# Kernel tuning notes

Measured on AMD Instinct MI355X. Metric: run time of the kernel, lower is better.

## Reference

```python
import jax, jax.numpy as jnp
import numpy as np

B, L, Q = 1024, 200, 1
DQ, DF = 512, 128
H, D1, D2 = 4, 128, 64


def setup_inputs() -> dict:
    key = jax.random.key(0)
    ks = jax.random.split(key, 20)
    inp = {
        "query": jax.random.normal(ks[0], (B, Q, DQ), jnp.float32),
        "fact": jax.random.normal(ks[1], (B, L, DF), jnp.float32),
        "mask": jax.random.randint(ks[2], (B, L), 0, 2, jnp.int32),
        "mm_cosine": jax.random.normal(ks[3], (2, B, L), jnp.float32),
    }
    # per-head FCRepeat weights, init per reset_parameters: randn/sqrt(fan_in), bias 0.1
    def w(k, fan_in, fan_out):
        return jax.random.normal(k, (H, fan_in, fan_out), jnp.float32) / np.sqrt(fan_in).astype(np.float32)
    inp["Wq1"] = w(ks[4], DQ, D1); inp["bq1"] = jnp.full((H, D1), 0.1, jnp.float32)
    inp["Wq2"] = w(ks[5], D1, D2); inp["bq2"] = jnp.full((H, D2), 0.1, jnp.float32)
    inp["Wf1"] = w(ks[6], DF, D1); inp["bf1"] = jnp.full((H, D1), 0.1, jnp.float32)
    inp["Wf2"] = w(ks[7], D1, D2); inp["bf2"] = jnp.full((H, D2), 0.1, jnp.float32)
    inp["Wv1"] = w(ks[8], DF, D1); inp["bv1"] = jnp.full((H, D1), 0.1, jnp.float32)
    inp["Wv2"] = w(ks[9], D1, D2); inp["bv2"] = jnp.full((H, D2), 0.1, jnp.float32)
    inp["tau1"] = jnp.full((2, H), 0.1, jnp.float32)   # cosine_tau1
    inp["tau2"] = jnp.full((3, H), 1.0, jnp.float32)   # cosine_tau2
    return inp


def _silu(x):
    return x * jax.nn.sigmoid(x)


def reference(query, fact, mask, mm_cosine,
              Wq1, bq1, Wq2, bq2, Wf1, bf1, Wf2, bf2, Wv1, bv1, Wv2, bv2,
              tau1, tau2):
    # per-head FC stacks (identity acts inside FCRepeat), then SiLU gating
    fq = jnp.einsum('bqi,hio->hbqo', query, Wq1) + bq1[:, None, None, :]
    fq = jnp.einsum('hbqi,hio->hbqo', fq, Wq2) + bq2[:, None, None, :]
    fq = _silu(fq)                                   # [H,B,1,D2]
    ff = jnp.einsum('bli,hio->hblo', fact, Wf1) + bf1[:, None, None, :]
    ff = jnp.einsum('hbli,hio->hblo', ff, Wf2) + bf2[:, None, None, :]
    ff = _silu(ff)                                   # [H,B,L,D2]
    fv = jnp.einsum('bli,hio->hblo', fact, Wv1) + bv1[:, None, None, :]
    fv = jnp.einsum('hbli,hio->hblo', fv, Wv2) + bv2[:, None, None, :]
    fv = _silu(fv)                                   # [H,B,L,D2]

    dot = jnp.einsum('hbld,hbqd->hblq', ff, fq)      # [H,B,L,1]
    dot = dot + (-1e9) * (1.0 - mask.astype(jnp.float32))[None, :, :, None]

    # cosine-bias cross terms
    bias = (mm_cosine[0][None] / tau1[0][:, None, None]
            + mm_cosine[1][None] / tau1[1][:, None, None])[..., None]  # [H,B,L,1]
    b1, b2, b3 = (tau2[i][:, None, None, None] for i in range(3))
    dot = b1 * dot + b2 * bias + b3 * dot * bias

    alphas = jax.nn.softmax(dot, axis=2) + 1e-7      # softmax over L
    out = jnp.einsum('hbld,hblq->hbdq', fv, alphas)[..., 0]  # [H,B,D2]
    return jnp.transpose(out, (1, 0, 2)).reshape(out.shape[1], -1)  # [B,H*D2]
```

## Files before the change

kernel.cpp:

```cpp
#include <hip/hip_runtime.h>
#include <hip/hip_bf16.h>

typedef __attribute__((ext_vector_type(8))) short short8;
typedef __attribute__((ext_vector_type(4))) float f32x4;

#define NH   4
#define NB   1024
#define NL   200
#define NDQ  512
#define NDF  128
#define ND1  128
#define ND2  64
#define LPAD 208
#define KP   136

#define OFF_WQC   0
#define OFF_BQC   (NH*NDQ*ND2*4)
#define OFF_FQ    (OFF_BQC + NH*ND2*4)
#define OFF_WIMG  (OFF_FQ + NH*NB*ND2*4)
#define OFF_BFC   (OFF_WIMG + NH*3*ND2*KP*2)
#define OFF_BVC   (OFF_BFC + NH*ND2*4)

__device__ inline short f2bf(float f) {
    union { float f; unsigned u; } v; v.f = f;
    unsigned r = (v.u + 0x7FFFu + ((v.u >> 16) & 1u)) >> 16;
    return (short)r;
}
__device__ inline float bf2f(short s) {
    union { unsigned u; float f; } v; v.u = ((unsigned)(unsigned short)s) << 16;
    return v.f;
}

__global__ __launch_bounds__(256) void k_combine(
    const float* __restrict__ Wq1, const float* __restrict__ bq1,
    const float* __restrict__ Wq2, const float* __restrict__ bq2,
    const float* __restrict__ Wf1, const float* __restrict__ bf1,
    const float* __restrict__ Wf2, const float* __restrict__ bf2,
    const float* __restrict__ Wv1, const float* __restrict__ bv1,
    const float* __restrict__ Wv2, const float* __restrict__ bv2,
    float* __restrict__ WQC, float* __restrict__ BQC,
    __hip_bfloat16* __restrict__ WIMG, float* __restrict__ BFC, float* __restrict__ BVC)
{
    int g = blockIdx.x * 256 + threadIdx.x;
    if (g < NH*NDQ*ND2) {
        int h = g >> 15, r = g & 32767, i = r >> 6, j = r & 63;
        const float* a  = Wq1 + (h*NDQ + i)*ND1;
        const float* bb = Wq2 + h*ND1*ND2 + j;
        float s = 0.f;
        for (int k = 0; k < ND1; ++k) s += a[k] * bb[k*ND2];
        WQC[(h*NDQ + i)*ND2 + j] = s;
        return;
    }
    g -= NH*NDQ*ND2;
    if (g < 2*NH*NDF*ND2) {
        int which = (g >= NH*NDF*ND2);
        int r0 = g & (NH*NDF*ND2 - 1);
        int h = r0 >> 13, r = r0 & 8191, i = r >> 6, j = r & 63;
        const float* W1 = (which ? Wv1 : Wf1) + (h*NDF + i)*ND1;
        const float* W2 = (which ? Wv2 : Wf2) + h*ND1*ND2 + j;
        float s = 0.f;
        for (int k = 0; k < ND1; ++k) s += W1[k] * W2[k*ND2];
        short hi = f2bf(s);
        short lo = f2bf(s - bf2f(hi));
        __hip_bfloat16* img = WIMG + (size_t)((h*3 + (which ? 2 : 0))*ND2 + j)*KP + i;
        ((short*)img)[0] = hi;
        if (!which) ((short*)img)[ND2*KP] = lo;
        return;
    }
    g -= 2*NH*NDF*ND2;
    if (g < NH*ND2) {
        int h = g >> 6, j = g & 63;
        float s = bq2[h*ND2 + j];
        for (int k = 0; k < ND1; ++k) s += bq1[h*ND1 + k] * Wq2[(h*ND1 + k)*ND2 + j];
        BQC[g] = s; return;
    }
    g -= NH*ND2;
    if (g < NH*ND2) {
        int h = g >> 6, j = g & 63;
        float s = bf2[h*ND2 + j];
        for (int k = 0; k < ND1; ++k) s += bf1[h*ND1 + k] * Wf2[(h*ND1 + k)*ND2 + j];
        BFC[g] = s; return;
    }
    g -= NH*ND2;
    if (g < NH*ND2) {
        int h = g >> 6, j = g & 63;
        float s = bv2[h*ND2 + j];
        for (int k = 0; k < ND1; ++k) s += bv1[h*ND1 + k] * Wv2[(h*ND1 + k)*ND2 + j];
        BVC[g] = s; return;
    }
}

__global__ __launch_bounds__(256) void k_fq(
    const float* __restrict__ query, const float* __restrict__ WQC,
    const float* __restrict__ BQC, float* __restrict__ FQ)
{
    __shared__ __align__(16) float qS[8*NDQ];
    const int t = threadIdx.x;
    const int b0 = blockIdx.x * 8;
    {
        const float4* src = (const float4*)(query + (size_t)b0 * NDQ);
        float4* dst = (float4*)qS;
        for (int i = t; i < 8*NDQ/4; i += 256) dst[i] = src[i];
    }
    __syncthreads();
    const int h = t >> 6, d = t & 63;
    float s[8];
    {
        float b = BQC[h*ND2 + d];
        for (int g = 0; g < 8; ++g) s[g] = b;
    }
    const float* wp = WQC + (size_t)h*NDQ*ND2 + d;
    for (int i = 0; i < NDQ; ++i) {
        float w = wp[i*ND2];
        for (int g = 0; g < 8; ++g) s[g] += qS[g*NDQ + i] * w;
    }
    for (int g = 0; g < 8; ++g) {
        float v = s[g];
        FQ[((size_t)h*NB + b0 + g)*ND2 + d] = v / (1.f + expf(-v));
    }
}

__global__ __launch_bounds__(512, 2) void k_main(
    const float* __restrict__ fact,
    const int* __restrict__ mask,
    const float* __restrict__ mmc,
    const float* __restrict__ tau1,
    const float* __restrict__ tau2,
    const float* __restrict__ FQ,
    const float* __restrict__ BFC,
    const float* __restrict__ BVC,
    const __hip_bfloat16* __restrict__ WIMG,
    float* __restrict__ out)
{
    __shared__ __align__(16) __hip_bfloat16 wS[2*ND2*KP];
    __shared__ __align__(16) float dotS[LPAD];
    __shared__ __align__(16) float alphaS[LPAD];
    __shared__ __align__(16) float redS[8];
    __shared__ __align__(16) float outPartS[512];

    const int t    = threadIdx.x;
    const int b    = blockIdx.x;
    const int w    = t >> 6;
    const int lane = t & 63;
    const int a15  = lane & 15;
    const int quad = lane >> 4;
    const int nmt  = (w < 5) ? 2 : 1;

    short8 afh[2][4], afl[2][4];
    const short8 zero8 = {0,0,0,0,0,0,0,0};
    for (int mi = 0; mi < 2; ++mi) {
        int mt = w + 8*mi;
        int row = mt*16 + a15;
        for (int kk = 0; kk < 4; ++kk) {
            short8 vh = zero8, vl = zero8;
            if (mt < 13 && row < NL) {
                const float* p = fact + ((size_t)(b*NL + row))*NDF + kk*32 + quad*8;
                float4 x0 = *(const float4*)p;
                float4 x1 = *(const float4*)(p + 4);
                float v[8] = {x0.x, x0.y, x0.z, x0.w, x1.x, x1.y, x1.z, x1.w};
                for (int j = 0; j < 8; ++j) {
                    short hs = f2bf(v[j]);
                    vh[j] = hs;
                    vl[j] = f2bf(v[j] - bf2f(hs));
                }
            }
            afh[mi][kk] = vh;
            afl[mi][kk] = vl;
        }
    }

    const int bL = b * NL;
    const f32x4 zf = {0.f, 0.f, 0.f, 0.f};

    for (int h = 0; h < NH; ++h) {
        __syncthreads();
        {
            const float4* src = (const float4*)(WIMG + (size_t)(h*3)*ND2*KP);
            float4* dst = (float4*)wS;
            for (int i = t; i < 2176; i += 512) dst[i] = src[i];
        }
        float fqv[4], bfcv[4], bvcv[4];
        for (int nt = 0; nt < 4; ++nt) {
            int col = nt*16 + a15;
            fqv[nt]  = FQ[((size_t)h*NB + b)*ND2 + col];
            bfcv[nt] = BFC[h*ND2 + col];
            bvcv[nt] = BVC[h*ND2 + col];
        }
        const float t1a = tau1[h];
        const float t1b = tau1[NH + h];
        const float t20 = tau2[h];
        const float t21 = tau2[NH + h];
        const float t22 = tau2[2*NH + h];
        __syncthreads();

        f32x4 acc[2][4];
        for (int mi = 0; mi < 2; ++mi) for (int nt = 0; nt < 4; ++nt) acc[mi][nt] = zf;
        for (int kk = 0; kk < 4; ++kk) {
            short8 bh[4], bl[4];
            for (int nt = 0; nt < 4; ++nt) {
                const __hip_bfloat16* p = wS + (nt*16 + a15)*KP + kk*32 + quad*8;
                bh[nt] = *(const short8*)p;
                bl[nt] = *(const short8*)(p + ND2*KP);
            }
            for (int mi = 0; mi < 2; ++mi)
                if (mi < nmt)
                    for (int nt = 0; nt < 4; ++nt) {
                        acc[mi][nt] = __builtin_amdgcn_mfma_f32_16x16x32_bf16(afh[mi][kk], bh[nt], acc[mi][nt], 0, 0, 0);
                        acc[mi][nt] = __builtin_amdgcn_mfma_f32_16x16x32_bf16(afh[mi][kk], bl[nt], acc[mi][nt], 0, 0, 0);
                        acc[mi][nt] = __builtin_amdgcn_mfma_f32_16x16x32_bf16(afl[mi][kk], bh[nt], acc[mi][nt], 0, 0, 0);
                    }
        }

        for (int mi = 0; mi < 2; ++mi)
            if (mi < nmt) {
                int mt = w + 8*mi;
                for (int rg = 0; rg < 4; ++rg) {
                    float s = 0.f;
                    for (int nt = 0; nt < 4; ++nt) {
                        float z = acc[mi][nt][rg] + bfcv[nt];
                        float ffv = z / (1.f + expf(-z));
                        s += ffv * fqv[nt];
                    }
                    s += __shfl_xor(s, 1);
                    s += __shfl_xor(s, 2);
                    s += __shfl_xor(s, 4);
                    s += __shfl_xor(s, 8);
                    if (a15 == rg) dotS[mt*16 + quad*4 + rg] = s;
                }
            }
        __syncthreads();

        {
            const float4* src = (const float4*)(WIMG + (size_t)(h*3 + 2)*ND2*KP);
            float4* dst = (float4*)wS;
            for (int i = t; i < 1088; i += 512) dst[i] = src[i];
        }

        float logit = -3.0e38f;
        float e = 0.f;
        if (t < NL) {
            float dv = dotS[t] - 1e9f * (1.0f - (float)mask[bL + t]);
            float bias = mmc[bL + t] / t1a + mmc[NB*NL + bL + t] / t1b;
            logit = t20*dv + t21*bias + t22*dv*bias;
        }
        float vmax = logit;
        for (int off = 1; off < 64; off <<= 1) vmax = fmaxf(vmax, __shfl_xor(vmax, off));
        if (lane == 0) redS[w] = vmax;
        __syncthreads();
        vmax = redS[0];
        for (int i = 1; i < 8; ++i) vmax = fmaxf(vmax, redS[i]);
        if (t < NL) e = expf(logit - vmax);
        float vsum = e;
        for (int off = 1; off < 64; off <<= 1) vsum += __shfl_xor(vsum, off);
        __syncthreads();
        if (lane == 0) redS[w] = vsum;
        __syncthreads();
        vsum = 0.f;
        for (int i = 0; i < 8; ++i) vsum += redS[i];
        if (t < LPAD) alphaS[t] = (t < NL) ? (e / vsum + 1e-7f) : 0.f;
        __syncthreads();

        for (int mi = 0; mi < 2; ++mi) for (int nt = 0; nt < 4; ++nt) acc[mi][nt] = zf;
        for (int kk = 0; kk < 4; ++kk) {
            short8 bh[4];
            for (int nt = 0; nt < 4; ++nt)
                bh[nt] = *(const short8*)(wS + (nt*16 + a15)*KP + kk*32 + quad*8);
            for (int mi = 0; mi < 2; ++mi)
                if (mi < nmt)
                    for (int nt = 0; nt < 4; ++nt)
                        acc[mi][nt] = __builtin_amdgcn_mfma_f32_16x16x32_bf16(afh[mi][kk], bh[nt], acc[mi][nt], 0, 0, 0);
        }

        float o[4] = {0.f, 0.f, 0.f, 0.f};
        for (int mi = 0; mi < 2; ++mi)
            if (mi < nmt) {
                int mt = w + 8*mi;
                const f32x4 al = *(const f32x4*)(alphaS + mt*16 + quad*4);
                for (int rg = 0; rg < 4; ++rg)
                    for (int nt = 0; nt < 4; ++nt) {
                        float z = acc[mi][nt][rg] + bvcv[nt];
                        float fvv = z / (1.f + expf(-z));
                        o[nt] += al[rg] * fvv;
                    }
            }
        for (int nt = 0; nt < 4; ++nt) {
            o[nt] += __shfl_xor(o[nt], 16);
            o[nt] += __shfl_xor(o[nt], 32);
        }
        if (lane < 16)
            for (int nt = 0; nt < 4; ++nt) outPartS[w*64 + nt*16 + lane] = o[nt];
        __syncthreads();
        if (t < 64) {
            float s = 0.f;
            for (int ww = 0; ww < 8; ++ww) s += outPartS[ww*64 + t];
            out[(size_t)b*(NH*ND2) + h*ND2 + t] = s;
        }
    }
}

extern "C" void kernel_launch(void* const* d_in, const int* in_sizes, int n_in,
                              void* d_out, int out_size, void* d_ws, size_t ws_size,
                              hipStream_t stream) {
    const float* query = (const float*)d_in[0];
    const float* fact  = (const float*)d_in[1];
    const int*   maskp = (const int*)d_in[2];
    const float* mmc   = (const float*)d_in[3];
    const float* Wq1 = (const float*)d_in[4];
    const float* bq1 = (const float*)d_in[5];
    const float* Wq2 = (const float*)d_in[6];
    const float* bq2 = (const float*)d_in[7];
    const float* Wf1 = (const float*)d_in[8];
    const float* bf1 = (const float*)d_in[9];
    const float* Wf2 = (const float*)d_in[10];
    const float* bf2 = (const float*)d_in[11];
    const float* Wv1 = (const float*)d_in[12];
    const float* bv1 = (const float*)d_in[13];
    const float* Wv2 = (const float*)d_in[14];
    const float* bv2 = (const float*)d_in[15];
    const float* tau1 = (const float*)d_in[16];
    const float* tau2 = (const float*)d_in[17];

    char* ws = (char*)d_ws;
    float*          WQC  = (float*)(ws + OFF_WQC);
    float*          BQC  = (float*)(ws + OFF_BQC);
    float*          FQ   = (float*)(ws + OFF_FQ);
    __hip_bfloat16* WIMG = (__hip_bfloat16*)(ws + OFF_WIMG);
    float*          BFC  = (float*)(ws + OFF_BFC);
    float*          BVC  = (float*)(ws + OFF_BVC);

    k_combine<<<771, 256, 0, stream>>>(Wq1, bq1, Wq2, bq2, Wf1, bf1, Wf2, bf2,
                                       Wv1, bv1, Wv2, bv2, WQC, BQC, WIMG, BFC, BVC);
    k_fq<<<NB/8, 256, 0, stream>>>(query, WQC, BQC, FQ);
    k_main<<<NB, 512, 0, stream>>>(fact, maskp, mmc, tau1, tau2, FQ, BFC, BVC, WIMG,
                                   (float*)d_out);
}
```

Baseline: 417.5 us.

## Cut barriers in main kernel by loading all weights once and wave-local softmax

```diff
diff --git a/kernel.cpp b/kernel.cpp
--- a/kernel.cpp
+++ b/kernel.cpp
@@ -29,6 +29,9 @@
 __device__ inline float bf2f(short s) {
     union { unsigned u; float f; } v; v.u = ((unsigned)(unsigned short)s) << 16;
     return v.f;
+}
+__device__ inline float fsilu(float z) {
+    return z * __fdividef(1.f, 1.f + __expf(-z));
 }
 
 __global__ __launch_bounds__(256) void k_combine(
@@ -94,30 +97,33 @@
     const float* __restrict__ query, const float* __restrict__ WQC,
     const float* __restrict__ BQC, float* __restrict__ FQ)
 {
-    __shared__ __align__(16) float qS[8*NDQ];
+    __shared__ __align__(16) float qS[4*NDQ];
     const int t = threadIdx.x;
-    const int b0 = blockIdx.x * 8;
+    const int b0 = blockIdx.x * 4;
     {
         const float4* src = (const float4*)(query + (size_t)b0 * NDQ);
         float4* dst = (float4*)qS;
-        for (int i = t; i < 8*NDQ/4; i += 256) dst[i] = src[i];
+        dst[t] = src[t];
+        dst[t + 256] = src[t + 256];
     }
     __syncthreads();
     const int h = t >> 6, d = t & 63;
-    float s[8];
-    {
-        float b = BQC[h*ND2 + d];
-        for (int g = 0; g < 8; ++g) s[g] = b;
-    }
+    float s0, s1, s2, s3;
+    s0 = s1 = s2 = s3 = BQC[h*ND2 + d];
     const float* wp = WQC + (size_t)h*NDQ*ND2 + d;
+    #pragma unroll 8
     for (int i = 0; i < NDQ; ++i) {
-        float w = wp[i*ND2];
-        for (int g = 0; g < 8; ++g) s[g] += qS[g*NDQ + i] * w;
-    }
-    for (int g = 0; g < 8; ++g) {
-        float v = s[g];
-        FQ[((size_t)h*NB + b0 + g)*ND2 + d] = v / (1.f + expf(-v));
-    }
+        float wv = wp[i*ND2];
+        s0 += qS[i]        * wv;
+        s1 += qS[NDQ + i]  * wv;
+        s2 += qS[2*NDQ + i]* wv;
+        s3 += qS[3*NDQ + i]* wv;
+    }
+    float* o = FQ + ((size_t)h*NB + b0)*ND2 + d;
+    o[0]      = fsilu(s0);
+    o[ND2]    = fsilu(s1);
+    o[2*ND2]  = fsilu(s2);
+    o[3*ND2]  = fsilu(s3);
 }
 
 __global__ __launch_bounds__(512, 2) void k_main(
@@ -132,10 +138,8 @@
     const __hip_bfloat16* __restrict__ WIMG,
     float* __restrict__ out)
 {
-    __shared__ __align__(16) __hip_bfloat16 wS[2*ND2*KP];
+    __shared__ __align__(16) __hip_bfloat16 wS[3*ND2*KP];
     __shared__ __align__(16) float dotS[LPAD];
-    __shared__ __align__(16) float alphaS[LPAD];
-    __shared__ __align__(16) float redS[8];
     __shared__ __align__(16) float outPartS[512];
 
     const int t    = threadIdx.x;
@@ -174,10 +178,15 @@
 
     for (int h = 0; h < NH; ++h) {
         __syncthreads();
+        if (h > 0 && t < 64) {
+            float s = 0.f;
+            for (int ww = 0; ww < 8; ++ww) s += outPartS[ww*64 + t];
+            out[(size_t)b*(NH*ND2) + (h-1)*ND2 + t] = s;
+        }
         {
             const float4* src = (const float4*)(WIMG + (size_t)(h*3)*ND2*KP);
             float4* dst = (float4*)wS;
-            for (int i = t; i < 2176; i += 512) dst[i] = src[i];
+            for (int i = t; i < 3264; i += 512) dst[i] = src[i];
         }
         float fqv[4], bfcv[4], bvcv[4];
         for (int nt = 0; nt < 4; ++nt) {
@@ -216,11 +225,8 @@
                 int mt = w + 8*mi;
                 for (int rg = 0; rg < 4; ++rg) {
                     float s = 0.f;
-                    for (int nt = 0; nt < 4; ++nt) {
-                        float z = acc[mi][nt][rg] + bfcv[nt];
-                        float ffv = z / (1.f + expf(-z));
-                        s += ffv * fqv[nt];
-                    }
+                    for (int nt = 0; nt < 4; ++nt)
+                        s += fsilu(acc[mi][nt][rg] + bfcv[nt]) * fqv[nt];
                     s += __shfl_xor(s, 1);
                     s += __shfl_xor(s, 2);
                     s += __shfl_xor(s, 4);
@@ -230,41 +236,51 @@
             }
         __syncthreads();
 
-        {
-            const float4* src = (const float4*)(WIMG + (size_t)(h*3 + 2)*ND2*KP);
-            float4* dst = (float4*)wS;
-            for (int i = t; i < 1088; i += 512) dst[i] = src[i];
-        }
-
-        float logit = -3.0e38f;
-        float e = 0.f;
-        if (t < NL) {
-            float dv = dotS[t] - 1e9f * (1.0f - (float)mask[bL + t]);
-            float bias = mmc[bL + t] / t1a + mmc[NB*NL + bL + t] / t1b;
-            logit = t20*dv + t21*bias + t22*dv*bias;
-        }
-        float vmax = logit;
+        float lg[4];
+        float vmax = -3.0e38f;
+        #pragma unroll
+        for (int j = 0; j < 4; ++j) {
+            int r = lane + 64*j;
+            float l = -3.0e38f;
+            if (r < NL) {
+                float dv = dotS[r] - 1e9f * (1.0f - (float)mask[bL + r]);
+                float bias = __fdividef(mmc[bL + r], t1a) + __fdividef(mmc[NB*NL + bL + r], t1b);
+                l = t20*dv + t21*bias + t22*dv*bias;
+            }
+            lg[j] = l;
+            vmax = fmaxf(vmax, l);
+        }
+        #pragma unroll
         for (int off = 1; off < 64; off <<= 1) vmax = fmaxf(vmax, __shfl_xor(vmax, off));
-        if (lane == 0) redS[w] = vmax;
-        __syncthreads();
-        vmax = redS[0];
-        for (int i = 1; i < 8; ++i) vmax = fmaxf(vmax, redS[i]);
-        if (t < NL) e = expf(logit - vmax);
-        float vsum = e;
+        float vsum = 0.f;
+        #pragma unroll
+        for (int j = 0; j < 4; ++j)
+            if (lane + 64*j < NL) vsum += __expf(lg[j] - vmax);
+        #pragma unroll
         for (int off = 1; off < 64; off <<= 1) vsum += __shfl_xor(vsum, off);
-        __syncthreads();
-        if (lane == 0) redS[w] = vsum;
-        __syncthreads();
-        vsum = 0.f;
-        for (int i = 0; i < 8; ++i) vsum += redS[i];
-        if (t < LPAD) alphaS[t] = (t < NL) ? (e / vsum + 1e-7f) : 0.f;
-        __syncthreads();
+        const float rdenom = __fdividef(1.f, vsum);
+
+        float al[2][4];
+        for (int mi = 0; mi < 2; ++mi)
+            for (int rg = 0; rg < 4; ++rg) {
+                float a = 0.f;
+                if (mi < nmt) {
+                    int r = (w + 8*mi)*16 + quad*4 + rg;
+                    if (r < NL) {
+                        float dv = dotS[r] - 1e9f * (1.0f - (float)mask[bL + r]);
+                        float bias = __fdividef(mmc[bL + r], t1a) + __fdividef(mmc[NB*NL + bL + r], t1b);
+                        float l = t20*dv + t21*bias + t22*dv*bias;
+                        a = __expf(l - vmax) * rdenom + 1e-7f;
+                    }
+                }
+                al[mi][rg] = a;
+            }
 
         for (int mi = 0; mi < 2; ++mi) for (int nt = 0; nt < 4; ++nt) acc[mi][nt] = zf;
         for (int kk = 0; kk < 4; ++kk) {
             short8 bh[4];
             for (int nt = 0; nt < 4; ++nt)
-                bh[nt] = *(const short8*)(wS + (nt*16 + a15)*KP + kk*32 + quad*8);
+                bh[nt] = *(const short8*)(wS + (2*ND2 + nt*16 + a15)*KP + kk*32 + quad*8);
             for (int mi = 0; mi < 2; ++mi)
                 if (mi < nmt)
                     for (int nt = 0; nt < 4; ++nt)
@@ -273,28 +289,22 @@
 
         float o[4] = {0.f, 0.f, 0.f, 0.f};
         for (int mi = 0; mi < 2; ++mi)
-            if (mi < nmt) {
-                int mt = w + 8*mi;
-                const f32x4 al = *(const f32x4*)(alphaS + mt*16 + quad*4);
+            if (mi < nmt)
                 for (int rg = 0; rg < 4; ++rg)
-                    for (int nt = 0; nt < 4; ++nt) {
-                        float z = acc[mi][nt][rg] + bvcv[nt];
-                        float fvv = z / (1.f + expf(-z));
-                        o[nt] += al[rg] * fvv;
-                    }
-            }
+                    for (int nt = 0; nt < 4; ++nt)
+                        o[nt] += al[mi][rg] * fsilu(acc[mi][nt][rg] + bvcv[nt]);
         for (int nt = 0; nt < 4; ++nt) {
             o[nt] += __shfl_xor(o[nt], 16);
             o[nt] += __shfl_xor(o[nt], 32);
         }
         if (lane < 16)
             for (int nt = 0; nt < 4; ++nt) outPartS[w*64 + nt*16 + lane] = o[nt];
-        __syncthreads();
-        if (t < 64) {
-            float s = 0.f;
-            for (int ww = 0; ww < 8; ++ww) s += outPartS[ww*64 + t];
-            out[(size_t)b*(NH*ND2) + h*ND2 + t] = s;
-        }
+    }
+    __syncthreads();
+    if (t < 64) {
+        float s = 0.f;
+        for (int ww = 0; ww < 8; ++ww) s += outPartS[ww*64 + t];
+        out[(size_t)b*(NH*ND2) + (NH-1)*ND2 + t] = s;
     }
 }
 
@@ -330,7 +340,7 @@
 
     k_combine<<<771, 256, 0, stream>>>(Wq1, bq1, Wq2, bq2, Wf1, bf1, Wf2, bf2,
                                        Wv1, bv1, Wv2, bv2, WQC, BQC, WIMG, BFC, BVC);
-    k_fq<<<NB/8, 256, 0, stream>>>(query, WQC, BQC, FQ);
+    k_fq<<<NB/4, 256, 0, stream>>>(query, WQC, BQC, FQ);
     k_main<<<NB, 512, 0, stream>>>(fact, maskp, mmc, tau1, tau2, FQ, BFC, BVC, WIMG,
                                    (float*)d_out);
 }
```

Result: faster. 383.8 us (-8.1%).
